# Performance work log

Measured on AMD Instinct MI355X. Metric: run time of the kernel, lower is better.

Reference implementation:

```python
import jax, jax.numpy as jnp
import numpy as np

B, L, H, N = 8, 2048, 512, 64  # batch, seq_len, d_model, SSM state size


def setup_inputs() -> dict:
    key = jax.random.key(0)
    ks = jax.random.split(key, 10)
    x = jax.random.normal(ks[0], (B, L, H), jnp.float32)
    # S4D-style parameters (diagonal SSM, S4D-Lin init)
    log_dt = jnp.log(1e-3) + jax.random.uniform(ks[1], (H,), jnp.float32) * (jnp.log(1e-1) - jnp.log(1e-3))
    A_re = -0.5 * jnp.ones((H, N), jnp.float32)
    A_im = jnp.tile(np.pi * jnp.arange(N, dtype=np.float32), (H, 1))
    C_re = jax.random.normal(ks[2], (H, N), jnp.float32) * (0.5 ** 0.5)
    C_im = jax.random.normal(ks[3], (H, N), jnp.float32) * (0.5 ** 0.5)
    D_skip = jax.random.normal(ks[4], (H,), jnp.float32)
    # S4 output linear (GLU): d_model -> 2*d_model, then gated
    W_out = jax.random.normal(ks[5], (2 * H, H), jnp.float32) / np.sqrt(H)
    b_out = jnp.zeros((2 * H,), jnp.float32)
    # LayerNorms
    g1 = jnp.ones((H,), jnp.float32); beta1 = jnp.zeros((H,), jnp.float32)
    g2 = jnp.ones((H,), jnp.float32); beta2 = jnp.zeros((H,), jnp.float32)
    # 1x1 conv FFN (kernel_size=1 => pointwise linear), d_ff = d_model
    W1 = jax.random.normal(ks[6], (H, H), jnp.float32) / np.sqrt(H)
    bc1 = jnp.zeros((H,), jnp.float32)
    W2 = jax.random.normal(ks[7], (H, H), jnp.float32) / np.sqrt(H)
    bc2 = jnp.zeros((H,), jnp.float32)
    return dict(x=x, log_dt=log_dt, A_re=A_re, A_im=A_im, C_re=C_re, C_im=C_im,
                D_skip=D_skip, W_out=W_out, b_out=b_out, g1=g1, beta1=beta1,
                g2=g2, beta2=beta2, W1=W1, bc1=bc1, W2=W2, bc2=bc2)


def _layer_norm(x, g, b):
    mu = jnp.mean(x, axis=-1, keepdims=True)
    var = jnp.mean((x - mu) ** 2, axis=-1, keepdims=True)
    return (x - mu) / jnp.sqrt(var + 1e-5) * g + b


def _s4(x, log_dt, A_re, A_im, C_re, C_im, D_skip, W_out, b_out):
    # x: (B, L, H) channels-last (transposed=False)
    Lx = x.shape[1]
    dt = jnp.exp(log_dt)                       # (H,)
    A = A_re + 1j * A_im                       # (H, N) diagonal state matrix
    dtA = A * dt[:, None]
    # ZOH discretization of C: Ct = C * (exp(dt*A) - 1) / A
    Ct = (C_re + 1j * C_im) * ((jnp.exp(dtA) - 1.0) / A)
    # Vandermonde kernel: K[h, l] = 2 Re sum_n Ct[h,n] exp(dt*A[h,n]*l)
    l = jnp.arange(Lx, dtype=jnp.float32)
    K = 2.0 * jnp.real(jnp.einsum('hn,hnl->hl', Ct, jnp.exp(dtA[:, :, None] * l)))
    # FFT long convolution (linear conv via zero-padded circular conv)
    u = jnp.swapaxes(x, 1, 2)                  # (B, H, L)
    n = 2 * Lx
    y = jnp.fft.irfft(jnp.fft.rfft(u, n) * jnp.fft.rfft(K, n)[None], n)[..., :Lx]
    y = y + D_skip[None, :, None] * u          # skip connection D*u
    y = jax.nn.gelu(y)                         # S4 default activation
    # output linear + GLU (S4 default postact)
    z = jnp.einsum('bhl,fh->bfl', y, W_out) + b_out[None, :, None]
    a, g = jnp.split(z, 2, axis=1)
    y = a * jax.nn.sigmoid(g)
    return jnp.swapaxes(y, 1, 2)               # (B, L, H)


def reference(x, log_dt, A_re, A_im, C_re, C_im, D_skip, W_out, b_out,
              g1, beta1, g2, beta2, W1, bc1, W2, bc2):
    new_x = _s4(x, log_dt, A_re, A_im, C_re, C_im, D_skip, W_out, b_out)
    x = x + new_x
    x = _layer_norm(x, g1, beta1)
    # FFN via 1x1 convs (pointwise linears); dropout is identity in eval
    y = jax.nn.relu(jnp.einsum('blh,fh->blf', x, W1) + bc1)
    y = jnp.einsum('blf,hf->blh', y, W2) + bc2
    return _layer_norm(x + y, g2, beta2)
```

## Files before the change

### kernel.cpp

```cpp
#include <hip/hip_runtime.h>
#include <cstddef>
#include <cstdint>

#define B_DIM 8
#define L_DIM 2048
#define H_DIM 512
#define N_DIM 64
#define HN (H_DIM * N_DIM)
#define BLH (B_DIM * L_DIM * H_DIM)
#define M_DIM (B_DIM * L_DIM)

typedef unsigned short u16;
typedef short bf16x8 __attribute__((ext_vector_type(8)));
typedef float floatx4 __attribute__((ext_vector_type(4)));

__device__ __forceinline__ float sigmoidf_(float v) {
    return 1.0f / (1.0f + __expf(-v));
}

__device__ __forceinline__ float gelu_tanh_(float x) {
    float x3 = x * x * x;
    float z = 0.7978845608028654f * fmaf(0.044715f, x3, x);
    float e = __expf(-2.0f * fabsf(z));
    float th = (1.0f - e) / (1.0f + e);
    th = copysignf(th, z);
    return 0.5f * x * (1.0f + th);
}

__device__ __forceinline__ u16 f2b(float f) {
    unsigned u = __float_as_uint(f);
    unsigned r = (u + 0x7fffu + ((u >> 16) & 1u)) >> 16;
    return (u16)r;
}
__device__ __forceinline__ float b2f(u16 u) {
    return __uint_as_float(((unsigned)u) << 16);
}
__device__ __forceinline__ void unpack2(unsigned u, float& a, float& b) {
    a = __uint_as_float(u << 16);
    b = __uint_as_float(u & 0xffff0000u);
}
__device__ __forceinline__ unsigned pack2(float a, float b) {
    return (unsigned)f2b(a) | ((unsigned)f2b(b) << 16);
}

__device__ __forceinline__ void csq(float& r, float& i) {
    float nr = r * r - i * i;
    i = 2.0f * r * i;
    r = nr;
}

__global__ __launch_bounds__(256) void cast_kernel(
    const float* __restrict__ src, u16* __restrict__ dst)
{
    int i = blockIdx.x * 256 + threadIdx.x;
    float4 v = *(const float4*)(src + (size_t)i * 4);
    uint2 p;
    p.x = pack2(v.x, v.y);
    p.y = pack2(v.z, v.w);
    *(uint2*)(dst + (size_t)i * 4) = p;
}

__global__ __launch_bounds__(256) void precompute_kernel(
    const float* __restrict__ log_dt, const float* __restrict__ A_re,
    const float* __restrict__ A_im, const float* __restrict__ C_re,
    const float* __restrict__ C_im, float* __restrict__ P)
{
    int i = blockIdx.x * 256 + threadIdx.x;
    if (i >= HN) return;
    int h = i >> 6;
    float dt = expf(log_dt[h]);
    float Ar = A_re[i], Ai = A_im[i];
    float ar = dt * Ar, ai = dt * Ai;
    float e = expf(ar);
    float wr = e * cosf(ai);
    float wi = e * sinf(ai);
    float em1r = wr - 1.0f, em1i = wi;
    float inv = 1.0f / fmaf(Ar, Ar, Ai * Ai);
    float qr = fmaf(em1r, Ar, em1i * Ai) * inv;
    float qi = fmaf(em1i, Ar, -(em1r * Ai)) * inv;
    float Cr = C_re[i], Ci = C_im[i];
    float ctr = Cr * qr - Ci * qi;
    float cti = Cr * qi + Ci * qr;
    P[i]          = wr;
    P[HN + i]     = wi;
    P[2 * HN + i] = 2.0f * ctr;
    P[3 * HN + i] = 2.0f * cti;
}

__global__ __launch_bounds__(256) void ktab_kernel(
    const float* __restrict__ P, float* __restrict__ Ktab)
{
    int wv = threadIdx.x >> 6, lane = threadIdx.x & 63;
    int h = blockIdx.x * 4 + wv;
    int pidx = (h << 6) + lane;
    float wr = P[pidx], wi = P[HN + pidx];
    float c2r = P[2 * HN + pidx], c2i = P[3 * HN + pidx];
    float pr = 1.0f, pi = 0.0f;
    for (int tau = 0; tau < 64; ++tau) {
        float term = c2r * pr - c2i * pi;
        #pragma unroll
        for (int m = 32; m > 0; m >>= 1) term += __shfl_xor(term, m, 64);
        if (lane == 0) Ktab[(h << 6) + tau] = term;
        float nr = pr * wr - pi * wi, ni = pr * wi + pi * wr;
        pr = nr; pi = ni;
    }
}

__global__ __launch_bounds__(256) void toepfill_kernel(
    const float* __restrict__ Ktab, u16* __restrict__ Toep_bf)
{
    int idx = blockIdx.x * 256 + threadIdx.x;
    int h = idx >> 12;
    int rem = idx & 4095;
    int tt = rem >> 6, j = rem & 63;
    u16 v = 0;
    if (j <= tt) v = f2b(Ktab[(h << 6) + (tt - j)]);
    Toep_bf[idx] = v;
}

__global__ __launch_bounds__(256) void xtrans_kernel(
    const float* __restrict__ x, u16* __restrict__ XT)
{
    __shared__ float tile[32][33];
    int b  = blockIdx.z;
    int l0 = blockIdx.x * 32;
    int h0 = blockIdx.y * 32;
    int tx = threadIdx.x & 31;
    int ty = threadIdx.x >> 5;
    #pragma unroll
    for (int r = 0; r < 4; ++r)
        tile[ty + r * 8][tx] = x[((size_t)b * L_DIM + l0 + ty + r * 8) * H_DIM + h0 + tx];
    __syncthreads();
    #pragma unroll
    for (int r = 0; r < 4; ++r)
        XT[((size_t)b * H_DIM + h0 + ty + r * 8) * L_DIM + l0 + tx] = f2b(tile[tx][ty + r * 8]);
}

__global__ __launch_bounds__(256) void ssm_chunk_kernel(
    const u16* __restrict__ XT, const float* __restrict__ P,
    const u16* __restrict__ Toep_bf, const float* __restrict__ D_skip,
    u16* __restrict__ YT)
{
    __shared__ u16 U[128 * 72];
    __shared__ u16 S[128 * 136];
    __shared__ u16 EVT[13312];
    u16* E  = EVT;
    u16* Tp = EVT;
    u16* V  = EVT + 4608;

    const int h    = blockIdx.x;
    const int b0   = blockIdx.y * 4;
    const int t    = threadIdx.x;
    const int lane = t & 63;
    const int wv   = t >> 6;
    const int lm   = lane & 15, lq = lane >> 4;

    const int pidx = (h << 6) + lane;
    const float wr  = P[pidx],          wi  = P[HN + pidx];
    const float c2r = P[2 * HN + pidx], c2i = P[3 * HN + pidx];

    #pragma unroll
    for (int r = 0; r < 4; ++r) {
        int idx = t + r * 256;
        int row = idx >> 3, ch = idx & 7;
        const u16* gp = XT + (((size_t)(b0 + (row >> 5)) * H_DIM + h) << 11)
                           + ((row & 31) << 6) + (ch << 3);
        *(uint4*)&U[row * 72 + ch * 8] = *(const uint4*)gp;
    }

    float bwr, bwi;
    {
        float g16r = wr, g16i = wi;
        csq(g16r, g16i); csq(g16r, g16i); csq(g16r, g16i); csq(g16r, g16i);
        if (wv == 0)      { bwr = 1.0f; bwi = 0.0f; }
        else if (wv == 1) { bwr = g16r; bwi = g16i; }
        else if (wv == 2) { bwr = g16r; bwi = g16i; csq(bwr, bwi); }
        else {
            float g32r = g16r, g32i = g16i; csq(g32r, g32i);
            bwr = g32r * g16r - g32i * g16i;
            bwi = g32r * g16i + g32i * g16r;
        }
    }

    {
        float pr = bwr, pi = bwi;
        #pragma unroll
        for (int jk = 0; jk < 16; ++jk) {
            int k = (wv << 4) + jk;
            int j = 63 - k;
            E[(2 * lane) * 72 + j]     = f2b(pr);
            E[(2 * lane + 1) * 72 + j] = f2b(pi);
            float nr = pr * wr - pi * wi, ni = pr * wi + pi * wr;
            pr = nr; pi = ni;
        }
    }
    __syncthreads();

    {
        const int wm = wv >> 1, wn = wv & 1;
        floatx4 acc[4][4] = {};
        #pragma unroll
        for (int ks = 0; ks < 2; ++ks) {
            bf16x8 af[4], bfv[4];
            #pragma unroll
            for (int i = 0; i < 4; ++i)
                af[i] = *(const bf16x8*)&E[(wm * 64 + i * 16 + lm) * 72 + ks * 32 + lq * 8];
            #pragma unroll
            for (int j = 0; j < 4; ++j)
                bfv[j] = *(const bf16x8*)&U[(wn * 64 + j * 16 + lm) * 72 + ks * 32 + lq * 8];
            #pragma unroll
            for (int i = 0; i < 4; ++i) {
                #pragma unroll
                for (int j = 0; j < 4; ++j)
                    acc[i][j] = __builtin_amdgcn_mfma_f32_16x16x32_bf16(af[i], bfv[j], acc[i][j], 0, 0, 0);
            }
        }
        #pragma unroll
        for (int i = 0; i < 4; ++i) {
            #pragma unroll
            for (int j = 0; j < 4; ++j) {
                int ncol = wn * 64 + j * 16 + lm;
                int m0   = wm * 64 + i * 16 + lq * 4;
                u16 pk[4];
                #pragma unroll
                for (int r = 0; r < 4; ++r) pk[r] = f2b(acc[i][j][r]);
                *(uint2*)&S[ncol * 136 + m0] = *(uint2*)pk;
            }
        }
    }
    __syncthreads();

    {
        float pr = bwr, pi = bwi;
        {
            float nr = pr * wr - pi * wi, ni = pr * wi + pi * wr;
            pr = nr; pi = ni;
        }
        #pragma unroll
        for (int jk = 1; jk <= 16; ++jk) {
            int tr = (wv << 4) + jk - 1;
            float qr = c2r * pr - c2i * pi;
            float qi = c2r * pi + c2i * pr;
            V[tr * 136 + 2 * lane]     = f2b(qr);
            V[tr * 136 + 2 * lane + 1] = f2b(-qi);
            float nr = pr * wr - pi * wi, ni = pr * wi + pi * wr;
            pr = nr; pi = ni;
        }
        #pragma unroll
        for (int r = 0; r < 2; ++r) {
            int idx = t + r * 256;
            int row = idx >> 3, ch = idx & 7;
            *(uint4*)&Tp[row * 72 + ch * 8] =
                *(const uint4*)&Toep_bf[((size_t)h << 12) + (row << 6) + (ch << 3)];
        }
        float wTr = wr, wTi = wi;
        csq(wTr, wTi); csq(wTr, wTi); csq(wTr, wTi);
        csq(wTr, wTi); csq(wTr, wTi); csq(wTr, wTi);
        float Sr = 0.0f, Si = 0.0f;
        const int n2 = lane * 2;
        for (int c = 0; c < 32; ++c) {
            int base = (wv * 32 + c) * 136 + n2;
            unsigned lv = *(unsigned*)&S[base];
            float lr, li;
            unpack2(lv, lr, li);
            *(unsigned*)&S[base] = pack2(Sr, Si);
            float nSr = wTr * Sr - wTi * Si + lr;
            Si = wTr * Si + wTi * Sr + li;
            Sr = nSr;
        }
    }
    __syncthreads();

    {
        const float Dh = D_skip[h];
        floatx4 acc[4][2] = {};
        #pragma unroll
        for (int ks = 0; ks < 6; ++ks) {
            bf16x8 af[4], bfv[2];
            if (ks < 2) {
                #pragma unroll
                for (int i = 0; i < 4; ++i)
                    af[i] = *(const bf16x8*)&Tp[(i * 16 + lm) * 72 + ks * 32 + lq * 8];
                #pragma unroll
                for (int j = 0; j < 2; ++j)
                    bfv[j] = *(const bf16x8*)&U[(wv * 32 + j * 16 + lm) * 72 + ks * 32 + lq * 8];
            } else {
                #pragma unroll
                for (int i = 0; i < 4; ++i)
                    af[i] = *(const bf16x8*)&V[(i * 16 + lm) * 136 + (ks - 2) * 32 + lq * 8];
                #pragma unroll
                for (int j = 0; j < 2; ++j)
                    bfv[j] = *(const bf16x8*)&S[(wv * 32 + j * 16 + lm) * 136 + (ks - 2) * 32 + lq * 8];
            }
            #pragma unroll
            for (int i = 0; i < 4; ++i) {
                #pragma unroll
                for (int j = 0; j < 2; ++j)
                    acc[i][j] = __builtin_amdgcn_mfma_f32_16x16x32_bf16(af[i], bfv[j], acc[i][j], 0, 0, 0);
            }
        }
        #pragma unroll
        for (int j = 0; j < 2; ++j) {
            int ncol = wv * 32 + j * 16 + lm;
            int bloc = ncol >> 5, c = ncol & 31;
            size_t gbase = (((size_t)(b0 + bloc) * H_DIM + h) << 11) + (c << 6);
            #pragma unroll
            for (int i = 0; i < 4; ++i) {
                int t0 = i * 16 + lq * 4;
                u16 upk[4];
                *(uint2*)upk = *(const uint2*)&U[ncol * 72 + t0];
                u16 opk[4];
                #pragma unroll
                for (int r = 0; r < 4; ++r) {
                    float uvv = b2f(upk[r]);
                    float yv = gelu_tanh_(fmaf(Dh, uvv, acc[i][j][r]));
                    opk[r] = f2b(yv);
                }
                *(uint2*)&YT[gbase + t0] = *(uint2*)opk;
            }
        }
    }
}

__global__ __launch_bounds__(256) void ytrans_kernel(
    const u16* __restrict__ YT, u16* __restrict__ Y)
{
    __shared__ u16 tile[32][33];
    int b  = blockIdx.z;
    int l0 = blockIdx.x * 32;
    int h0 = blockIdx.y * 32;
    int tx = threadIdx.x & 31;
    int ty = threadIdx.x >> 5;
    #pragma unroll
    for (int r = 0; r < 4; ++r)
        tile[ty + r * 8][tx] = YT[((size_t)b * H_DIM + h0 + ty + r * 8) * L_DIM + l0 + tx];
    __syncthreads();
    #pragma unroll
    for (int r = 0; r < 4; ++r)
        Y[((size_t)b * L_DIM + l0 + ty + r * 8) * H_DIM + h0 + tx] = tile[tx][ty + r * 8];
}

__device__ __forceinline__ void stage_tile_128x64(
    const u16* __restrict__ g, u16* lds, int row0, int k0)
{
    const int t = threadIdx.x;
    #pragma unroll
    for (int r = 0; r < 4; ++r) {
        int idx  = t + r * 256;
        int row  = idx >> 3;
        int cs   = idx & 7;
        int csrc = cs ^ (row & 7);
        const u16* gp = g + (size_t)(row0 + row) * 512 + k0 + csrc * 8;
        __builtin_amdgcn_global_load_lds(
            (const __attribute__((address_space(1))) unsigned int*)gp,
            (__attribute__((address_space(3))) unsigned int*)(lds + (size_t)idx * 8),
            16, 0, 0);
    }
}

__device__ __forceinline__ bf16x8 ldfrag(const u16* lds, int row, int cc)
{
    int p = cc ^ (row & 7);
    return *(const bf16x8*)&lds[row * 64 + p * 8];
}

__global__ __launch_bounds__(256) void gemm1_glu_kernel(
    const u16* __restrict__ A, const u16* __restrict__ Wo,
    const float* __restrict__ bo, const float* __restrict__ x,
    u16* __restrict__ out)
{
    __shared__ u16 As[128 * 64];
    __shared__ u16 Ba[128 * 64];
    __shared__ u16 Bg[128 * 64];
    const int t    = threadIdx.x;
    const int lane = t & 63;
    const int wv   = t >> 6;
    const int wm   = wv >> 1, wn = wv & 1;
    const int lm   = lane & 15, lq = lane >> 4;
    const int m0   = blockIdx.x * 128, n0 = blockIdx.y * 128;
    floatx4 accA[4][4] = {};
    floatx4 accG[4][4] = {};
    for (int k0 = 0; k0 < 512; k0 += 64) {
        stage_tile_128x64(A, As, m0, k0);
        stage_tile_128x64(Wo, Ba, n0, k0);
        stage_tile_128x64(Wo, Bg, 512 + n0, k0);
        __syncthreads();
        #pragma unroll
        for (int ks = 0; ks < 2; ++ks) {
            bf16x8 af[4], ba[4], bg[4];
            #pragma unroll
            for (int i = 0; i < 4; ++i)
                af[i] = ldfrag(As, wm * 64 + i * 16 + lm, ks * 4 + lq);
            #pragma unroll
            for (int j = 0; j < 4; ++j) {
                ba[j] = ldfrag(Ba, wn * 64 + j * 16 + lm, ks * 4 + lq);
                bg[j] = ldfrag(Bg, wn * 64 + j * 16 + lm, ks * 4 + lq);
            }
            #pragma unroll
            for (int i = 0; i < 4; ++i) {
                #pragma unroll
                for (int j = 0; j < 4; ++j) {
                    accA[i][j] = __builtin_amdgcn_mfma_f32_16x16x32_bf16(ba[j], af[i], accA[i][j], 0, 0, 0);
                    accG[i][j] = __builtin_amdgcn_mfma_f32_16x16x32_bf16(bg[j], af[i], accG[i][j], 0, 0, 0);
                }
            }
        }
        __syncthreads();
    }
    #pragma unroll
    for (int i = 0; i < 4; ++i) {
        int m = m0 + wm * 64 + i * 16 + lm;
        #pragma unroll
        for (int j = 0; j < 4; ++j) {
            int n = n0 + wn * 64 + j * 16 + lq * 4;
            float4 ba4 = *(const float4*)&bo[n];
            float4 bg4 = *(const float4*)&bo[512 + n];
            float4 xv  = *(const float4*)&x[(size_t)m * 512 + n];
            const float* baf = (const float*)&ba4;
            const float* bgf = (const float*)&bg4;
            const float* xf  = (const float*)&xv;
            u16 pk[4];
            #pragma unroll
            for (int r = 0; r < 4; ++r) {
                float av = accA[i][j][r] + baf[r];
                float gv = accG[i][j][r] + bgf[r];
                pk[r] = f2b(fmaf(av, sigmoidf_(gv), xf[r]));
            }
            *(uint2*)&out[(size_t)m * 512 + n] = *(uint2*)pk;
        }
    }
}

template<int EPI>
__global__ __launch_bounds__(256) void gemm_bt_bf_kernel(
    const u16* __restrict__ A, const u16* __restrict__ Bw,
    const float* __restrict__ bias, u16* __restrict__ C)
{
    __shared__ u16 As[128 * 64];
    __shared__ u16 Bs[128 * 64];
    const int t    = threadIdx.x;
    const int lane = t & 63;
    const int wv   = t >> 6;
    const int wm   = wv >> 1, wn = wv & 1;
    const int lm   = lane & 15, lq = lane >> 4;
    const int m0   = blockIdx.x * 128, n0 = blockIdx.y * 128;
    floatx4 acc[4][4] = {};
    for (int k0 = 0; k0 < 512; k0 += 64) {
        stage_tile_128x64(A, As, m0, k0);
        stage_tile_128x64(Bw, Bs, n0, k0);
        __syncthreads();
        #pragma unroll
        for (int ks = 0; ks < 2; ++ks) {
            bf16x8 af[4], bfr[4];
            #pragma unroll
            for (int i = 0; i < 4; ++i)
                af[i] = ldfrag(As, wm * 64 + i * 16 + lm, ks * 4 + lq);
            #pragma unroll
            for (int j = 0; j < 4; ++j)
                bfr[j] = ldfrag(Bs, wn * 64 + j * 16 + lm, ks * 4 + lq);
            #pragma unroll
            for (int i = 0; i < 4; ++i) {
                #pragma unroll
                for (int j = 0; j < 4; ++j)
                    acc[i][j] = __builtin_amdgcn_mfma_f32_16x16x32_bf16(bfr[j], af[i], acc[i][j], 0, 0, 0);
            }
        }
        __syncthreads();
    }
    #pragma unroll
    for (int i = 0; i < 4; ++i) {
        int m = m0 + wm * 64 + i * 16 + lm;
        #pragma unroll
        for (int j = 0; j < 4; ++j) {
            int n = n0 + wn * 64 + j * 16 + lq * 4;
            float4 bv4 = *(const float4*)&bias[n];
            const float* bvf = (const float*)&bv4;
            u16 pk[4];
            #pragma unroll
            for (int r = 0; r < 4; ++r) {
                float v = acc[i][j][r] + bvf[r];
                if (EPI == 1) v = fmaxf(v, 0.0f);
                pk[r] = f2b(v);
            }
            *(uint2*)&C[(size_t)m * 512 + n] = *(uint2*)pk;
        }
    }
}

template<bool HASRES, bool F32OUT>
__global__ __launch_bounds__(256) void ln_bf_kernel(
    const u16* __restrict__ in, const u16* __restrict__ res,
    const float* __restrict__ gamma, const float* __restrict__ beta,
    u16* __restrict__ outb, float* __restrict__ outf)
{
    int w    = threadIdx.x >> 6;
    int lane = threadIdx.x & 63;
    size_t row  = (size_t)blockIdx.x * 4 + w;
    size_t base = row * 512 + lane * 8;
    uint4 raw = *(const uint4*)(in + base);
    float v[8];
    unpack2(raw.x, v[0], v[1]); unpack2(raw.y, v[2], v[3]);
    unpack2(raw.z, v[4], v[5]); unpack2(raw.w, v[6], v[7]);
    if (HASRES) {
        uint4 rr = *(const uint4*)(res + base);
        float rv[8];
        unpack2(rr.x, rv[0], rv[1]); unpack2(rr.y, rv[2], rv[3]);
        unpack2(rr.z, rv[4], rv[5]); unpack2(rr.w, rv[6], rv[7]);
        #pragma unroll
        for (int i = 0; i < 8; ++i) v[i] += rv[i];
    }
    float s = 0.0f, sq = 0.0f;
    #pragma unroll
    for (int i = 0; i < 8; ++i) { s += v[i]; sq = fmaf(v[i], v[i], sq); }
    #pragma unroll
    for (int m = 32; m > 0; m >>= 1) {
        s  += __shfl_xor(s, m, 64);
        sq += __shfl_xor(sq, m, 64);
    }
    float mu  = s * (1.0f / 512.0f);
    float var = sq * (1.0f / 512.0f) - mu * mu;
    float rs  = rsqrtf(var + 1e-5f);
    float g[8], bt[8];
    *(float4*)&g[0]  = *(const float4*)(gamma + lane * 8);
    *(float4*)&g[4]  = *(const float4*)(gamma + lane * 8 + 4);
    *(float4*)&bt[0] = *(const float4*)(beta + lane * 8);
    *(float4*)&bt[4] = *(const float4*)(beta + lane * 8 + 4);
    float o[8];
    #pragma unroll
    for (int i = 0; i < 8; ++i)
        o[i] = fmaf((v[i] - mu) * rs, g[i], bt[i]);
    if (F32OUT) {
        *(float4*)(outf + base)     = *(float4*)&o[0];
        *(float4*)(outf + base + 4) = *(float4*)&o[4];
    } else {
        uint4 p;
        p.x = pack2(o[0], o[1]); p.y = pack2(o[2], o[3]);
        p.z = pack2(o[4], o[5]); p.w = pack2(o[6], o[7]);
        *(uint4*)(outb + base) = p;
    }
}

extern "C" void kernel_launch(void* const* d_in, const int* in_sizes, int n_in,
                              void* d_out, int out_size, void* d_ws, size_t ws_size,
                              hipStream_t stream)
{
    (void)in_sizes; (void)n_in; (void)out_size; (void)ws_size;
    const float* x      = (const float*)d_in[0];
    const float* log_dt = (const float*)d_in[1];
    const float* A_re   = (const float*)d_in[2];
    const float* A_im   = (const float*)d_in[3];
    const float* C_re   = (const float*)d_in[4];
    const float* C_im   = (const float*)d_in[5];
    const float* D_skip = (const float*)d_in[6];
    const float* W_out  = (const float*)d_in[7];
    const float* b_out  = (const float*)d_in[8];
    const float* g1     = (const float*)d_in[9];
    const float* beta1  = (const float*)d_in[10];
    const float* g2     = (const float*)d_in[11];
    const float* beta2  = (const float*)d_in[12];
    const float* W1     = (const float*)d_in[13];
    const float* bc1    = (const float*)d_in[14];
    const float* W2     = (const float*)d_in[15];
    const float* bc2    = (const float*)d_in[16];
    float* out = (float*)d_out;

    char*  wsb    = (char*)d_ws;
    float* P      = (float*)wsb;
    float* Ktab   = (float*)(wsb + 4 * HN * 4);
    u16*   Toep   = (u16*)(wsb + 4 * HN * 4 + 512 * 64 * 4);
    u16*   Wobf   = Toep + 512 * 4096;
    u16*   W1bf   = Wobf + 1024 * 512;
    u16*   W2bf   = W1bf + 512 * 512;
    u16*   r1     = W2bf + 512 * 512;
    u16*   r2     = r1 + BLH;
    u16*   r3     = r2 + BLH;

    cast_kernel<<<512, 256, 0, stream>>>(W_out, Wobf);
    cast_kernel<<<256, 256, 0, stream>>>(W1, W1bf);
    cast_kernel<<<256, 256, 0, stream>>>(W2, W2bf);
    precompute_kernel<<<HN / 256, 256, 0, stream>>>(log_dt, A_re, A_im, C_re, C_im, P);
    ktab_kernel<<<128, 256, 0, stream>>>(P, Ktab);
    toepfill_kernel<<<8192, 256, 0, stream>>>(Ktab, Toep);
    xtrans_kernel<<<dim3(L_DIM / 32, H_DIM / 32, B_DIM), 256, 0, stream>>>(x, r1);
    ssm_chunk_kernel<<<dim3(H_DIM, 2), 256, 0, stream>>>(r1, P, Toep, D_skip, r2);
    ytrans_kernel<<<dim3(L_DIM / 32, H_DIM / 32, B_DIM), 256, 0, stream>>>(r2, r3);
    gemm1_glu_kernel<<<dim3(M_DIM / 128, 4), 256, 0, stream>>>(r3, Wobf, b_out, x, r2);
    ln_bf_kernel<false, false><<<M_DIM / 4, 256, 0, stream>>>(r2, nullptr, g1, beta1, r1, nullptr);
    gemm_bt_bf_kernel<1><<<dim3(M_DIM / 128, 4), 256, 0, stream>>>(r1, W1bf, bc1, r3);
    gemm_bt_bf_kernel<0><<<dim3(M_DIM / 128, 4), 256, 0, stream>>>(r3, W2bf, bc2, r2);
    ln_bf_kernel<true, true><<<M_DIM / 4, 256, 0, stream>>>(r2, r1, g2, beta2, nullptr, out);
}
```

Baseline: 269.9 us.

## Fuse LayerNorm1, FFN GEMMs and LayerNorm2 into one kernel; drop LDS staging in GLU GEMM

The two FFN GEMMs and both LayerNorms now run in a single kernel that handles 32 rows per block. It keeps the normalized input and the hidden activations in swizzled LDS, so intermediates no longer round-trip through global memory and three launches are removed. The GLU GEMM switches from LDS-staged 128x128 tiles to 64-row tiles whose fragments are loaded straight from global memory, with no barriers. In exchange, each block rereads the full weight matrices from global memory or cache with less reuse per block, and the small 32-row tiles lower MFMA efficiency.

```diff
diff --git a/kernel.cpp b/kernel.cpp
--- a/kernel.cpp
+++ b/kernel.cpp
@@ -340,79 +340,54 @@
         Y[((size_t)b * L_DIM + l0 + ty + r * 8) * H_DIM + h0 + tx] = tile[tx][ty + r * 8];
 }
 
-__device__ __forceinline__ void stage_tile_128x64(
-    const u16* __restrict__ g, u16* lds, int row0, int k0)
-{
-    const int t = threadIdx.x;
-    #pragma unroll
-    for (int r = 0; r < 4; ++r) {
-        int idx  = t + r * 256;
-        int row  = idx >> 3;
-        int cs   = idx & 7;
-        int csrc = cs ^ (row & 7);
-        const u16* gp = g + (size_t)(row0 + row) * 512 + k0 + csrc * 8;
-        __builtin_amdgcn_global_load_lds(
-            (const __attribute__((address_space(1))) unsigned int*)gp,
-            (__attribute__((address_space(3))) unsigned int*)(lds + (size_t)idx * 8),
-            16, 0, 0);
-    }
-}
-
-__device__ __forceinline__ bf16x8 ldfrag(const u16* lds, int row, int cc)
-{
-    int p = cc ^ (row & 7);
-    return *(const bf16x8*)&lds[row * 64 + p * 8];
-}
-
 __global__ __launch_bounds__(256) void gemm1_glu_kernel(
-    const u16* __restrict__ A, const u16* __restrict__ Wo,
+    const u16* __restrict__ Y, const u16* __restrict__ Wo,
     const float* __restrict__ bo, const float* __restrict__ x,
     u16* __restrict__ out)
 {
-    __shared__ u16 As[128 * 64];
-    __shared__ u16 Ba[128 * 64];
-    __shared__ u16 Bg[128 * 64];
-    const int t    = threadIdx.x;
-    const int lane = t & 63;
-    const int wv   = t >> 6;
-    const int wm   = wv >> 1, wn = wv & 1;
+    const int lane = threadIdx.x & 63;
+    const int wv   = threadIdx.x >> 6;
     const int lm   = lane & 15, lq = lane >> 4;
-    const int m0   = blockIdx.x * 128, n0 = blockIdx.y * 128;
-    floatx4 accA[4][4] = {};
-    floatx4 accG[4][4] = {};
-    for (int k0 = 0; k0 < 512; k0 += 64) {
-        stage_tile_128x64(A, As, m0, k0);
-        stage_tile_128x64(Wo, Ba, n0, k0);
-        stage_tile_128x64(Wo, Bg, 512 + n0, k0);
-        __syncthreads();
+    const int m0   = blockIdx.x * 64;
+    const int n0   = blockIdx.y * 128;
+    const int nw   = n0 + wv * 32;
+
+    floatx4 accA[4][2] = {};
+    floatx4 accG[4][2] = {};
+    #pragma unroll
+    for (int kq = 0; kq < 8; ++kq) {
+        bf16x8 af[2][4], ba[2][2], bg[2][2];
         #pragma unroll
         for (int ks = 0; ks < 2; ++ks) {
-            bf16x8 af[4], ba[4], bg[4];
+            int kk = kq * 64 + ks * 32 + lq * 8;
             #pragma unroll
             for (int i = 0; i < 4; ++i)
-                af[i] = ldfrag(As, wm * 64 + i * 16 + lm, ks * 4 + lq);
-            #pragma unroll
-            for (int j = 0; j < 4; ++j) {
-                ba[j] = ldfrag(Ba, wn * 64 + j * 16 + lm, ks * 4 + lq);
-                bg[j] = ldfrag(Bg, wn * 64 + j * 16 + lm, ks * 4 + lq);
-            }
+                af[ks][i] = *(const bf16x8*)&Y[(size_t)(m0 + i * 16 + lm) * 512 + kk];
+            #pragma unroll
+            for (int j = 0; j < 2; ++j) {
+                int n = nw + j * 16 + lm;
+                ba[ks][j] = *(const bf16x8*)&Wo[(size_t)n * 512 + kk];
+                bg[ks][j] = *(const bf16x8*)&Wo[(size_t)(512 + n) * 512 + kk];
+            }
+        }
+        #pragma unroll
+        for (int ks = 0; ks < 2; ++ks) {
             #pragma unroll
             for (int i = 0; i < 4; ++i) {
                 #pragma unroll
-                for (int j = 0; j < 4; ++j) {
-                    accA[i][j] = __builtin_amdgcn_mfma_f32_16x16x32_bf16(ba[j], af[i], accA[i][j], 0, 0, 0);
-                    accG[i][j] = __builtin_amdgcn_mfma_f32_16x16x32_bf16(bg[j], af[i], accG[i][j], 0, 0, 0);
+                for (int j = 0; j < 2; ++j) {
+                    accA[i][j] = __builtin_amdgcn_mfma_f32_16x16x32_bf16(ba[ks][j], af[ks][i], accA[i][j], 0, 0, 0);
+                    accG[i][j] = __builtin_amdgcn_mfma_f32_16x16x32_bf16(bg[ks][j], af[ks][i], accG[i][j], 0, 0, 0);
                 }
             }
         }
-        __syncthreads();
     }
     #pragma unroll
     for (int i = 0; i < 4; ++i) {
-        int m = m0 + wm * 64 + i * 16 + lm;
-        #pragma unroll
-        for (int j = 0; j < 4; ++j) {
-            int n = n0 + wn * 64 + j * 16 + lq * 4;
+        int m = m0 + i * 16 + lm;
+        #pragma unroll
+        for (int j = 0; j < 2; ++j) {
+            int n = nw + j * 16 + lq * 4;
             float4 ba4 = *(const float4*)&bo[n];
             float4 bg4 = *(const float4*)&bo[512 + n];
             float4 xv  = *(const float4*)&x[(size_t)m * 512 + n];
@@ -431,112 +406,210 @@
     }
 }
 
-template<int EPI>
-__global__ __launch_bounds__(256) void gemm_bt_bf_kernel(
-    const u16* __restrict__ A, const u16* __restrict__ Bw,
-    const float* __restrict__ bias, u16* __restrict__ C)
-{
-    __shared__ u16 As[128 * 64];
-    __shared__ u16 Bs[128 * 64];
+__global__ __launch_bounds__(256) void ffn_fused_kernel(
+    const u16* __restrict__ X1, const u16* __restrict__ W1bf,
+    const float* __restrict__ b1v, const u16* __restrict__ W2bf,
+    const float* __restrict__ b2v,
+    const float* __restrict__ ga1, const float* __restrict__ be1,
+    const float* __restrict__ ga2, const float* __restrict__ be2,
+    float* __restrict__ out)
+{
+    __shared__ u16 XN[32 * 512];
+    __shared__ u16 H1[32 * 512];
     const int t    = threadIdx.x;
     const int lane = t & 63;
     const int wv   = t >> 6;
-    const int wm   = wv >> 1, wn = wv & 1;
     const int lm   = lane & 15, lq = lane >> 4;
-    const int m0   = blockIdx.x * 128, n0 = blockIdx.y * 128;
-    floatx4 acc[4][4] = {};
-    for (int k0 = 0; k0 < 512; k0 += 64) {
-        stage_tile_128x64(A, As, m0, k0);
-        stage_tile_128x64(Bw, Bs, n0, k0);
-        __syncthreads();
-        #pragma unroll
-        for (int ks = 0; ks < 2; ++ks) {
-            bf16x8 af[4], bfr[4];
-            #pragma unroll
-            for (int i = 0; i < 4; ++i)
-                af[i] = ldfrag(As, wm * 64 + i * 16 + lm, ks * 4 + lq);
-            #pragma unroll
-            for (int j = 0; j < 4; ++j)
-                bfr[j] = ldfrag(Bs, wn * 64 + j * 16 + lm, ks * 4 + lq);
-            #pragma unroll
-            for (int i = 0; i < 4; ++i) {
-                #pragma unroll
-                for (int j = 0; j < 4; ++j)
-                    acc[i][j] = __builtin_amdgcn_mfma_f32_16x16x32_bf16(bfr[j], af[i], acc[i][j], 0, 0, 0);
-            }
-        }
-        __syncthreads();
-    }
-    #pragma unroll
-    for (int i = 0; i < 4; ++i) {
-        int m = m0 + wm * 64 + i * 16 + lm;
-        #pragma unroll
-        for (int j = 0; j < 4; ++j) {
-            int n = n0 + wn * 64 + j * 16 + lq * 4;
-            float4 bv4 = *(const float4*)&bias[n];
-            const float* bvf = (const float*)&bv4;
-            u16 pk[4];
-            #pragma unroll
-            for (int r = 0; r < 4; ++r) {
-                float v = acc[i][j][r] + bvf[r];
-                if (EPI == 1) v = fmaxf(v, 0.0f);
-                pk[r] = f2b(v);
-            }
-            *(uint2*)&C[(size_t)m * 512 + n] = *(uint2*)pk;
-        }
-    }
-}
-
-template<bool HASRES, bool F32OUT>
-__global__ __launch_bounds__(256) void ln_bf_kernel(
-    const u16* __restrict__ in, const u16* __restrict__ res,
-    const float* __restrict__ gamma, const float* __restrict__ beta,
-    u16* __restrict__ outb, float* __restrict__ outf)
-{
-    int w    = threadIdx.x >> 6;
-    int lane = threadIdx.x & 63;
-    size_t row  = (size_t)blockIdx.x * 4 + w;
-    size_t base = row * 512 + lane * 8;
-    uint4 raw = *(const uint4*)(in + base);
-    float v[8];
-    unpack2(raw.x, v[0], v[1]); unpack2(raw.y, v[2], v[3]);
-    unpack2(raw.z, v[4], v[5]); unpack2(raw.w, v[6], v[7]);
-    if (HASRES) {
-        uint4 rr = *(const uint4*)(res + base);
-        float rv[8];
-        unpack2(rr.x, rv[0], rv[1]); unpack2(rr.y, rv[2], rv[3]);
-        unpack2(rr.z, rv[4], rv[5]); unpack2(rr.w, rv[6], rv[7]);
-        #pragma unroll
-        for (int i = 0; i < 8; ++i) v[i] += rv[i];
-    }
-    float s = 0.0f, sq = 0.0f;
-    #pragma unroll
-    for (int i = 0; i < 8; ++i) { s += v[i]; sq = fmaf(v[i], v[i], sq); }
-    #pragma unroll
-    for (int m = 32; m > 0; m >>= 1) {
-        s  += __shfl_xor(s, m, 64);
-        sq += __shfl_xor(sq, m, 64);
-    }
-    float mu  = s * (1.0f / 512.0f);
-    float var = sq * (1.0f / 512.0f) - mu * mu;
-    float rs  = rsqrtf(var + 1e-5f);
-    float g[8], bt[8];
-    *(float4*)&g[0]  = *(const float4*)(gamma + lane * 8);
-    *(float4*)&g[4]  = *(const float4*)(gamma + lane * 8 + 4);
-    *(float4*)&bt[0] = *(const float4*)(beta + lane * 8);
-    *(float4*)&bt[4] = *(const float4*)(beta + lane * 8 + 4);
-    float o[8];
-    #pragma unroll
-    for (int i = 0; i < 8; ++i)
-        o[i] = fmaf((v[i] - mu) * rs, g[i], bt[i]);
-    if (F32OUT) {
-        *(float4*)(outf + base)     = *(float4*)&o[0];
-        *(float4*)(outf + base + 4) = *(float4*)&o[4];
-    } else {
-        uint4 p;
-        p.x = pack2(o[0], o[1]); p.y = pack2(o[2], o[3]);
-        p.z = pack2(o[4], o[5]); p.w = pack2(o[6], o[7]);
-        *(uint4*)(outb + base) = p;
+    const int m0   = blockIdx.x * 32;
+
+    #pragma unroll
+    for (int r = 0; r < 8; ++r) {
+        int idx = t + r * 256;
+        int row = idx >> 6, cs = idx & 63;
+        int cc  = (cs & ~7) | ((cs & 7) ^ (row & 7));
+        const u16* gp = X1 + (size_t)(m0 + row) * 512 + cc * 8;
+        __builtin_amdgcn_global_load_lds(
+            (const __attribute__((address_space(1))) unsigned int*)gp,
+            (__attribute__((address_space(3))) unsigned int*)(XN + (size_t)idx * 8),
+            16, 0, 0);
+    }
+    __syncthreads();
+
+    {
+        float g[8], bb[8];
+        *(float4*)&g[0]  = *(const float4*)(ga1 + lane * 8);
+        *(float4*)&g[4]  = *(const float4*)(ga1 + lane * 8 + 4);
+        *(float4*)&bb[0] = *(const float4*)(be1 + lane * 8);
+        *(float4*)&bb[4] = *(const float4*)(be1 + lane * 8 + 4);
+        #pragma unroll
+        for (int rr = 0; rr < 8; ++rr) {
+            int row  = wv * 8 + rr;
+            int slot = (lane & ~7) | ((lane & 7) ^ (row & 7));
+            u16* p = &XN[row * 512 + slot * 8];
+            uint4 raw = *(const uint4*)p;
+            float v[8];
+            unpack2(raw.x, v[0], v[1]); unpack2(raw.y, v[2], v[3]);
+            unpack2(raw.z, v[4], v[5]); unpack2(raw.w, v[6], v[7]);
+            float s = 0.0f, sq = 0.0f;
+            #pragma unroll
+            for (int i = 0; i < 8; ++i) { s += v[i]; sq = fmaf(v[i], v[i], sq); }
+            #pragma unroll
+            for (int m = 32; m > 0; m >>= 1) {
+                s  += __shfl_xor(s, m, 64);
+                sq += __shfl_xor(sq, m, 64);
+            }
+            float mu  = s * (1.0f / 512.0f);
+            float var = sq * (1.0f / 512.0f) - mu * mu;
+            float rs  = rsqrtf(var + 1e-5f);
+            uint4 pk;
+            pk.x = pack2(fmaf((v[0]-mu)*rs, g[0], bb[0]), fmaf((v[1]-mu)*rs, g[1], bb[1]));
+            pk.y = pack2(fmaf((v[2]-mu)*rs, g[2], bb[2]), fmaf((v[3]-mu)*rs, g[3], bb[3]));
+            pk.z = pack2(fmaf((v[4]-mu)*rs, g[4], bb[4]), fmaf((v[5]-mu)*rs, g[5], bb[5]));
+            pk.w = pack2(fmaf((v[6]-mu)*rs, g[6], bb[6]), fmaf((v[7]-mu)*rs, g[7], bb[7]));
+            *(uint4*)p = pk;
+        }
+    }
+    __syncthreads();
+
+    #pragma unroll
+    for (int nt = 0; nt < 4; ++nt) {
+        floatx4 acc[2][2] = {};
+        #pragma unroll
+        for (int kq = 0; kq < 8; ++kq) {
+            bf16x8 af[2][2], wf[2][2];
+            #pragma unroll
+            for (int ks = 0; ks < 2; ++ks) {
+                #pragma unroll
+                for (int i = 0; i < 2; ++i) {
+                    int row  = i * 16 + lm;
+                    int slot = kq * 8 + ((ks * 4 + lq) ^ (row & 7));
+                    af[ks][i] = *(const bf16x8*)&XN[row * 512 + slot * 8];
+                }
+                #pragma unroll
+                for (int j = 0; j < 2; ++j) {
+                    int n = nt * 128 + wv * 32 + j * 16 + lm;
+                    wf[ks][j] = *(const bf16x8*)&W1bf[(size_t)n * 512 + kq * 64 + ks * 32 + lq * 8];
+                }
+            }
+            #pragma unroll
+            for (int ks = 0; ks < 2; ++ks)
+                #pragma unroll
+                for (int i = 0; i < 2; ++i)
+                    #pragma unroll
+                    for (int j = 0; j < 2; ++j)
+                        acc[i][j] = __builtin_amdgcn_mfma_f32_16x16x32_bf16(wf[ks][j], af[ks][i], acc[i][j], 0, 0, 0);
+        }
+        #pragma unroll
+        for (int i = 0; i < 2; ++i) {
+            int m = i * 16 + lm;
+            #pragma unroll
+            for (int j = 0; j < 2; ++j) {
+                int n = nt * 128 + wv * 32 + j * 16 + lq * 4;
+                float4 b4 = *(const float4*)&b1v[n];
+                const float* bf4 = (const float*)&b4;
+                u16 pk[4];
+                #pragma unroll
+                for (int r = 0; r < 4; ++r)
+                    pk[r] = f2b(fmaxf(acc[i][j][r] + bf4[r], 0.0f));
+                int cc   = n >> 3;
+                int slot = (cc & ~7) | ((cc & 7) ^ (m & 7));
+                *(uint2*)&H1[m * 512 + slot * 8 + (n & 7)] = *(uint2*)pk;
+            }
+        }
+    }
+    __syncthreads();
+
+    floatx4 acc2[4][2][2] = {};
+    #pragma unroll
+    for (int nt = 0; nt < 4; ++nt) {
+        #pragma unroll
+        for (int kq = 0; kq < 8; ++kq) {
+            bf16x8 af[2][2], wf[2][2];
+            #pragma unroll
+            for (int ks = 0; ks < 2; ++ks) {
+                #pragma unroll
+                for (int i = 0; i < 2; ++i) {
+                    int row  = i * 16 + lm;
+                    int slot = kq * 8 + ((ks * 4 + lq) ^ (row & 7));
+                    af[ks][i] = *(const bf16x8*)&H1[row * 512 + slot * 8];
+                }
+                #pragma unroll
+                for (int j = 0; j < 2; ++j) {
+                    int n = nt * 128 + wv * 32 + j * 16 + lm;
+                    wf[ks][j] = *(const bf16x8*)&W2bf[(size_t)n * 512 + kq * 64 + ks * 32 + lq * 8];
+                }
+            }
+            #pragma unroll
+            for (int ks = 0; ks < 2; ++ks)
+                #pragma unroll
+                for (int i = 0; i < 2; ++i)
+                    #pragma unroll
+                    for (int j = 0; j < 2; ++j)
+                        acc2[nt][i][j] = __builtin_amdgcn_mfma_f32_16x16x32_bf16(wf[ks][j], af[ks][i], acc2[nt][i][j], 0, 0, 0);
+        }
+    }
+    __syncthreads();
+
+    #pragma unroll
+    for (int nt = 0; nt < 4; ++nt) {
+        #pragma unroll
+        for (int i = 0; i < 2; ++i) {
+            int m = i * 16 + lm;
+            #pragma unroll
+            for (int j = 0; j < 2; ++j) {
+                int n = nt * 128 + wv * 32 + j * 16 + lq * 4;
+                float4 b4 = *(const float4*)&b2v[n];
+                const float* bf4 = (const float*)&b4;
+                u16 pk[4];
+                #pragma unroll
+                for (int r = 0; r < 4; ++r)
+                    pk[r] = f2b(acc2[nt][i][j][r] + bf4[r]);
+                int cc   = n >> 3;
+                int slot = (cc & ~7) | ((cc & 7) ^ (m & 7));
+                *(uint2*)&H1[m * 512 + slot * 8 + (n & 7)] = *(uint2*)pk;
+            }
+        }
+    }
+    __syncthreads();
+
+    {
+        float g[8], bb[8];
+        *(float4*)&g[0]  = *(const float4*)(ga2 + lane * 8);
+        *(float4*)&g[4]  = *(const float4*)(ga2 + lane * 8 + 4);
+        *(float4*)&bb[0] = *(const float4*)(be2 + lane * 8);
+        *(float4*)&bb[4] = *(const float4*)(be2 + lane * 8 + 4);
+        #pragma unroll
+        for (int rr = 0; rr < 8; ++rr) {
+            int row  = wv * 8 + rr;
+            int slot = (lane & ~7) | ((lane & 7) ^ (row & 7));
+            uint4 ry = *(const uint4*)&H1[row * 512 + slot * 8];
+            uint4 rx = *(const uint4*)&XN[row * 512 + slot * 8];
+            float v[8], xv[8];
+            unpack2(ry.x, v[0], v[1]); unpack2(ry.y, v[2], v[3]);
+            unpack2(ry.z, v[4], v[5]); unpack2(ry.w, v[6], v[7]);
+            unpack2(rx.x, xv[0], xv[1]); unpack2(rx.y, xv[2], xv[3]);
+            unpack2(rx.z, xv[4], xv[5]); unpack2(rx.w, xv[6], xv[7]);
+            #pragma unroll
+            for (int i = 0; i < 8; ++i) v[i] += xv[i];
+            float s = 0.0f, sq = 0.0f;
+            #pragma unroll
+            for (int i = 0; i < 8; ++i) { s += v[i]; sq = fmaf(v[i], v[i], sq); }
+            #pragma unroll
+            for (int m = 32; m > 0; m >>= 1) {
+                s  += __shfl_xor(s, m, 64);
+                sq += __shfl_xor(sq, m, 64);
+            }
+            float mu  = s * (1.0f / 512.0f);
+            float var = sq * (1.0f / 512.0f) - mu * mu;
+            float rs  = rsqrtf(var + 1e-5f);
+            float o[8];
+            #pragma unroll
+            for (int i = 0; i < 8; ++i)
+                o[i] = fmaf((v[i] - mu) * rs, g[i], bb[i]);
+            size_t gbase = (size_t)(m0 + row) * 512 + lane * 8;
+            *(float4*)(out + gbase)     = *(float4*)&o[0];
+            *(float4*)(out + gbase + 4) = *(float4*)&o[4];
+        }
     }
 }
 
@@ -584,9 +657,7 @@
     xtrans_kernel<<<dim3(L_DIM / 32, H_DIM / 32, B_DIM), 256, 0, stream>>>(x, r1);
     ssm_chunk_kernel<<<dim3(H_DIM, 2), 256, 0, stream>>>(r1, P, Toep, D_skip, r2);
     ytrans_kernel<<<dim3(L_DIM / 32, H_DIM / 32, B_DIM), 256, 0, stream>>>(r2, r3);
-    gemm1_glu_kernel<<<dim3(M_DIM / 128, 4), 256, 0, stream>>>(r3, Wobf, b_out, x, r2);
-    ln_bf_kernel<false, false><<<M_DIM / 4, 256, 0, stream>>>(r2, nullptr, g1, beta1, r1, nullptr);
-    gemm_bt_bf_kernel<1><<<dim3(M_DIM / 128, 4), 256, 0, stream>>>(r1, W1bf, bc1, r3);
-    gemm_bt_bf_kernel<0><<<dim3(M_DIM / 128, 4), 256, 0, stream>>>(r3, W2bf, bc2, r2);
-    ln_bf_kernel<true, true><<<M_DIM / 4, 256, 0, stream>>>(r2, r1, g2, beta2, nullptr, out);
-}
+    gemm1_glu_kernel<<<dim3(M_DIM / 64, 4), 256, 0, stream>>>(r3, Wobf, b_out, x, r2);
+    ffn_fused_kernel<<<M_DIM / 32, 256, 0, stream>>>(r2, W1bf, bc1, W2bf, bc2,
+                                                     g1, beta1, g2, beta2, out);
+}
```

Result: slower. 329.8 us (+22.2%).
